# Kernel optimization log

Hardware: AMD Instinct MI355X
Metric: run time of the kernel (lower is better)

## Reference

```python
import jax, jax.numpy as jnp
import numpy as np

B, T, F, H = 16, 1024, 1024, 16
D = F // H  # 64

def setup_inputs() -> dict:
    key = jax.random.key(0)
    k0, k1, k2 = jax.random.split(key, 3)
    return {
        "x": jax.random.normal(k0, (B, T, F), jnp.float32),
        "mask": jnp.zeros((B, 1, T, 1), jnp.float32),
        "W_attn": jax.random.normal(k1, (F, 3 * F), jnp.float32) * 0.02,
        "b_attn": jnp.zeros((3 * F,), jnp.float32),
        "W_proj": jax.random.normal(k2, (F, F), jnp.float32) * 0.02,
        "b_proj": jnp.zeros((F,), jnp.float32),
    }

def reference(x, mask, W_attn, b_attn, W_proj, b_proj):
    # qkv projection (Conv1D == linear with transposed weight layout)
    qkv = x @ W_attn + b_attn                       # [B,T,3F]
    q, k, v = jnp.split(qkv, 3, axis=-1)
    split = lambda t: t.reshape(B, T, H, D).transpose(0, 2, 1, 3)  # [B,H,T,D]
    q, k, v = split(q), split(k), split(v)
    # non-standard: contract over T -> [B,H,D,D] score matrix
    s = jnp.einsum('bhtd,bhte->bhde', q, k) / jnp.sqrt(jnp.float32(D))
    tril = jnp.tril(jnp.ones((D, D), bool))         # bias buffer sliced to DxD
    s = jnp.where(tril, s, jnp.float32(-10000.0))
    # second matmul with V (before softmax), scaled by dk^2
    w = jnp.einsum('bhde,bhte->bhtd', s, v) / (jnp.float32(D) ** 2)  # [B,H,T,D]
    w = jax.nn.softmax(w + mask, axis=-2)           # softmax over T (dim=-2)
    a = w * v                                        # elementwise, not weighted sum
    merge = lambda t: t.transpose(0, 2, 1, 3).reshape(B, T, F)
    a = merge(a) @ W_proj + b_proj                   # output projection
    return a, merge(w)
```

## Files before the change

### kernel.cpp

```cpp
#include <hip/hip_runtime.h>
#include <math.h>

namespace {
constexpr int B = 16, T = 1024, F = 1024, H = 16, D = 64;
constexpr int NT = B * T;
constexpr int QKV_COLS = 3 * F;

constexpr size_t XHI_OFF = 0;
constexpr size_t XLO_OFF = 33554432;
constexpr size_t WAH_OFF = 67108864;
constexpr size_t WVL_OFF = 73400320;
constexpr size_t QB_OFF  = 75497472;
constexpr size_t KB_OFF  = 109051904;
constexpr size_t SB_OFF  = 142606336;
constexpr size_t AB_OFF  = 146800640;
constexpr size_t WPB_OFF = 180355072;
constexpr size_t VB_OFF   = QB_OFF;
constexpr size_t SP_OFF   = WVL_OFF;
}

typedef __attribute__((ext_vector_type(8))) __bf16 bf16x8;
typedef __attribute__((ext_vector_type(4))) float f32x4;

__device__ __forceinline__ unsigned short f2bf(float f) {
  unsigned u = __builtin_bit_cast(unsigned, f);
  u += 0x7FFFu + ((u >> 16) & 1u);
  return (unsigned short)(u >> 16);
}
__device__ __forceinline__ float bf2f(unsigned short s) {
  return __builtin_bit_cast(float, (unsigned)s << 16);
}
__device__ __forceinline__ void gld16(const unsigned short* g, unsigned short* l) {
  __builtin_amdgcn_global_load_lds(
      (const __attribute__((address_space(1))) unsigned int*)g,
      (__attribute__((address_space(3))) unsigned int*)l, 16, 0, 0);
}

__global__ __launch_bounds__(256) void cast_x(const float* __restrict__ x,
                                              unsigned short* __restrict__ xhi,
                                              unsigned short* __restrict__ xlo) {
  int i = (blockIdx.x * 256 + threadIdx.x) * 4;
  float4 v = *(const float4*)&x[i];
  ushort4 h, l;
  h.x = f2bf(v.x); l.x = f2bf(v.x - bf2f(h.x));
  h.y = f2bf(v.y); l.y = f2bf(v.y - bf2f(h.y));
  h.z = f2bf(v.z); l.z = f2bf(v.z - bf2f(h.z));
  h.w = f2bf(v.w); l.w = f2bf(v.w - bf2f(h.w));
  *(ushort4*)&xhi[i] = h;
  *(ushort4*)&xlo[i] = l;
}

__global__ __launch_bounds__(256) void tcast(const float* __restrict__ W,
                                             unsigned short* __restrict__ Wt,
                                             unsigned short* __restrict__ Wlo,
                                             int ncols, int locol0) {
  __shared__ float tile[64][65];
  const int bx = blockIdx.x, by = blockIdx.y, tid = threadIdx.x;
#pragma unroll
  for (int i = 0; i < 16; ++i) {
    int idx = tid + i * 256;
    int r = idx >> 6, c = idx & 63;
    tile[r][c] = W[(size_t)(by * 64 + r) * ncols + bx * 64 + c];
  }
  __syncthreads();
#pragma unroll
  for (int i = 0; i < 16; ++i) {
    int idx = tid + i * 256;
    int r = idx >> 6, c = idx & 63;
    int col = bx * 64 + r;
    float w = tile[c][r];
    unsigned short h = f2bf(w);
    Wt[(size_t)col * 1024 + by * 64 + c] = h;
    if (col >= locol0) {
      Wlo[(size_t)(col - locol0) * 1024 + by * 64 + c] = f2bf(w - bf2f(h));
    }
  }
}

__device__ __forceinline__ void stage256(const unsigned short* __restrict__ Ag,
                                         const unsigned short* __restrict__ Bg,
                                         int row0, int col0, int kin,
                                         unsigned short* lbase, int wave,
                                         int lane) {
  const int rsub = lane >> 3;
  const int logb = ((lane & 7) ^ rsub) << 4;
  const int isB = logb >> 6;
  const int koff = kin + ((logb & 63) >> 1);
#pragma unroll
  for (int L = 0; L < 4; ++L) {
    const int R0 = (L * 8 + wave) * 8;
    const int r = R0 + rsub;
    const unsigned short* src =
        isB ? (Bg + (size_t)(col0 + r) * 1024 + koff)
            : (Ag + (size_t)(row0 + r) * 1024 + koff);
    gld16(src, lbase + (size_t)R0 * 64);
  }
}

template <int MODE>
__device__ __forceinline__ void tile_src(
    int kt, const unsigned short* __restrict__ A0,
    const unsigned short* __restrict__ A1,
    const unsigned short* __restrict__ B0,
    const unsigned short* __restrict__ B1,
    const unsigned short*& Ag, const unsigned short*& Bg, int& kin) {
  if constexpr (MODE == 1) {
    const int seg = kt >> 5;
    kin = (kt & 31) << 5;
    Ag = (seg == 1) ? A1 : A0;
    Bg = (seg == 2) ? B1 : B0;
  } else {
    Ag = A0; Bg = B0; kin = kt << 5;
  }
}

__device__ __forceinline__ void read_frags(const char* tb, int wr, int wc,
                                           int m16, int quad,
                                           bf16x8 (&dst)[12]) {
#pragma unroll
  for (int j = 0; j < 4; ++j) {
    const int c = wc * 64 + j * 16 + m16;
    dst[j] = *(const bf16x8*)(tb + c * 128 +
                              ((64 + quad * 16) ^ ((c & 7) << 4)));
  }
#pragma unroll
  for (int i = 0; i < 8; ++i) {
    const int r = wr * 128 + i * 16 + m16;
    dst[4 + i] = *(const bf16x8*)(tb + r * 128 +
                                  ((quad * 16) ^ ((r & 7) << 4)));
  }
}

template <int MODE, int VM, bool STG, bool RDN>
__device__ __forceinline__ void half_body(
    int j, int row0, int col0, const unsigned short* __restrict__ A0,
    const unsigned short* __restrict__ A1,
    const unsigned short* __restrict__ B0,
    const unsigned short* __restrict__ B1,
    unsigned short (*lds)[256][64], int wave, int lane, int wr, int wc,
    int m16, int quad, bf16x8 (&cur)[12], bf16x8 (&nxt)[12],
    f32x4 (&acc)[8][4]) {
  if constexpr (STG) {
    const unsigned short *Ag, *Bg; int kin;
    tile_src<MODE>(j + 3, A0, A1, B0, B1, Ag, Bg, kin);
    stage256(Ag, Bg, row0, col0, kin, &lds[(j + 3) & 3][0][0], wave, lane);
  }
  if constexpr (VM == 8)      asm volatile("s_waitcnt vmcnt(8)" ::: "memory");
  else if constexpr (VM == 4) asm volatile("s_waitcnt vmcnt(4)" ::: "memory");
  else if constexpr (VM == 0) asm volatile("s_waitcnt vmcnt(0)" ::: "memory");
  __builtin_amdgcn_s_barrier();
  __builtin_amdgcn_sched_barrier(0);
  if constexpr (RDN) {
    read_frags((const char*)&lds[(j + 1) & 3][0][0], wr, wc, m16, quad, nxt);
  }
  __builtin_amdgcn_s_setprio(1);
#pragma unroll
  for (int i = 0; i < 8; ++i)
#pragma unroll
    for (int jj = 0; jj < 4; ++jj)
      acc[i][jj] = __builtin_amdgcn_mfma_f32_16x16x32_bf16(
          cur[4 + i], cur[jj], acc[i][jj], 0, 0, 0);
  __builtin_amdgcn_s_setprio(0);
  __builtin_amdgcn_s_barrier();
  __builtin_amdgcn_sched_barrier(0);
}

template <int MODE>
__global__ __launch_bounds__(512, 2) void gemm256(
    const unsigned short* __restrict__ A0, const unsigned short* __restrict__ A1,
    const unsigned short* __restrict__ B0, const unsigned short* __restrict__ B1,
    const float* __restrict__ bias, void* __restrict__ out0,
    void* __restrict__ out1) {
  __shared__ __align__(16) unsigned short lds[4][256][64];
  const int tid = threadIdx.x;
  const int wave = tid >> 6, lane = tid & 63;
  const int wr = wave >> 2, wc = wave & 3;
  const int m16 = lane & 15, quad = lane >> 4;
  const int row0 = blockIdx.y * 256, col0 = blockIdx.x * 256;
  constexpr int NKT = (MODE == 1) ? 96 : 32;
  f32x4 acc[8][4] = {};
  bf16x8 s0[12], s1[12];

#pragma unroll
  for (int p = 0; p < 3; ++p) {
    const unsigned short *Ag, *Bg; int kin;
    tile_src<MODE>(p, A0, A1, B0, B1, Ag, Bg, kin);
    stage256(Ag, Bg, row0, col0, kin, &lds[p][0][0], wave, lane);
  }
  asm volatile("s_waitcnt vmcnt(8)" ::: "memory");
  __builtin_amdgcn_s_barrier();
  __builtin_amdgcn_sched_barrier(0);
  read_frags((const char*)&lds[0][0][0], wr, wc, m16, quad, s0);

  int kt = 0;
  for (; kt + 5 < NKT; kt += 2) {
    half_body<MODE, 8, true, true>(kt, row0, col0, A0, A1, B0, B1, lds, wave,
                                   lane, wr, wc, m16, quad, s0, s1, acc);
    half_body<MODE, 8, true, true>(kt + 1, row0, col0, A0, A1, B0, B1, lds,
                                   wave, lane, wr, wc, m16, quad, s1, s0, acc);
  }
  half_body<MODE, 8, true, true>(NKT - 4, row0, col0, A0, A1, B0, B1, lds,
                                 wave, lane, wr, wc, m16, quad, s0, s1, acc);
  half_body<MODE, 4, false, true>(NKT - 3, row0, col0, A0, A1, B0, B1, lds,
                                  wave, lane, wr, wc, m16, quad, s1, s0, acc);
  half_body<MODE, 0, false, true>(NKT - 2, row0, col0, A0, A1, B0, B1, lds,
                                  wave, lane, wr, wc, m16, quad, s0, s1, acc);
  half_body<MODE, -1, false, false>(NKT - 1, row0, col0, A0, A1, B0, B1, lds,
                                    wave, lane, wr, wc, m16, quad, s1, s0, acc);

  if constexpr (MODE == 0) {
    unsigned short* dst = (col0 >= 1024) ? (unsigned short*)out1
                                         : (unsigned short*)out0;
#pragma unroll
    for (int j = 0; j < 4; ++j) {
      const int gcol = col0 + wc * 64 + j * 16 + m16;
      const int f = gcol & 1023;
      const int h = f >> 6, dd = f & 63;
      const float bv = bias[gcol];
#pragma unroll
      for (int i = 0; i < 8; ++i) {
#pragma unroll
        for (int r = 0; r < 4; ++r) {
          const int grow = row0 + wr * 128 + i * 16 + quad * 4 + r;
          const int b = grow >> 10, t = grow & 1023;
          dst[(((size_t)b * H + h) * T + t) * D + dd] = f2bf(acc[i][j][r] + bv);
        }
      }
    }
  } else if constexpr (MODE == 1) {
    float* vbp = (float*)out0;
#pragma unroll
    for (int j = 0; j < 4; ++j) {
      const int f = col0 + wc * 64 + j * 16 + m16;
      const int h = f >> 6, dd = f & 63;
      const float bv = bias[f];
#pragma unroll
      for (int i = 0; i < 8; ++i) {
#pragma unroll
        for (int r = 0; r < 4; ++r) {
          const int grow = row0 + wr * 128 + i * 16 + quad * 4 + r;
          const int b = grow >> 10, t = grow & 1023;
          vbp[(((size_t)b * H + h) * T + t) * D + dd] = acc[i][j][r] + bv;
        }
      }
    }
  } else {
    float* o = (float*)out0;
#pragma unroll
    for (int j = 0; j < 4; ++j) {
      const int gcol = col0 + wc * 64 + j * 16 + m16;
      const float bv = bias[gcol];
#pragma unroll
      for (int i = 0; i < 8; ++i) {
#pragma unroll
        for (int r = 0; r < 4; ++r) {
          const int grow = row0 + wr * 128 + i * 16 + quad * 4 + r;
          o[(size_t)grow * F + gcol] = acc[i][j][r] + bv;
        }
      }
    }
  }
}

__global__ __launch_bounds__(256) void score_kernel(
    const unsigned short* __restrict__ qb, const unsigned short* __restrict__ kb,
    float* __restrict__ sb) {
  __shared__ float qs[64][68];
  __shared__ float ks[64][68];
  const int bh = blockIdx.x;
  const int tid = threadIdx.x;
  const size_t base = (size_t)bh * T * D;
  const int d0 = (tid >> 4) * 4, e0 = (tid & 15) * 4;
  float acc[4][4] = {};
  for (int ch = 0; ch < T / 64; ++ch) {
#pragma unroll
    for (int i = 0; i < 4; ++i) {
      int idx = (tid + i * 256) * 4;
      ushort4 qv = *(const ushort4*)&qb[base + (size_t)ch * 4096 + idx];
      ushort4 kv = *(const ushort4*)&kb[base + (size_t)ch * 4096 + idx];
      int r = idx >> 6, c = idx & 63;
      float4 qf = make_float4(bf2f(qv.x), bf2f(qv.y), bf2f(qv.z), bf2f(qv.w));
      float4 kf = make_float4(bf2f(kv.x), bf2f(kv.y), bf2f(kv.z), bf2f(kv.w));
      *(float4*)&qs[r][c] = qf;
      *(float4*)&ks[r][c] = kf;
    }
    __syncthreads();
#pragma unroll 8
    for (int tt = 0; tt < 64; ++tt) {
      float4 qa4 = *(const float4*)&qs[tt][d0];
      float4 kv4 = *(const float4*)&ks[tt][e0];
      float qa[4] = {qa4.x, qa4.y, qa4.z, qa4.w};
      float kv[4] = {kv4.x, kv4.y, kv4.z, kv4.w};
#pragma unroll
      for (int i = 0; i < 4; ++i)
#pragma unroll
        for (int j = 0; j < 4; ++j) acc[i][j] += qa[i] * kv[j];
    }
    __syncthreads();
  }
#pragma unroll
  for (int i = 0; i < 4; ++i) {
#pragma unroll
    for (int j = 0; j < 4; ++j) {
      int dd = d0 + i, ee = e0 + j;
      float v = acc[i][j] * 0.125f;
      if (ee > dd) v = -10000.0f;
      sb[(size_t)bh * (D * D) + dd * D + ee] = v;
    }
  }
}

__global__ __launch_bounds__(256) void sum_kernel(
    const float* __restrict__ vb, const float* __restrict__ sb,
    const float* __restrict__ mask, float* __restrict__ sp) {
  const int tc = blockIdx.x, bh = blockIdx.y;
  const int b = bh >> 4;
  const int tid = threadIdx.x;
  const int lane = tid & 63;
  const int dg = __builtin_amdgcn_readfirstlane(tid >> 6);
  const int tg = tc * 64 + lane;
  const float* vrow = vb + (size_t)bh * (T * D) + (size_t)tg * D;
  float4 vreg[16];
#pragma unroll
  for (int i = 0; i < 16; ++i) vreg[i] = *(const float4*)&vrow[i * 4];
  const float mval = mask[(size_t)b * T + tg];
  float ex[16];
#pragma unroll
  for (int dd = 0; dd < 16; ++dd) {
    const int d = dg * 16 + dd;
    const float* srow = sb + (size_t)bh * 4096 + (size_t)d * 64;
    float acc = 0.f;
#pragma unroll
    for (int e4 = 0; e4 < 16; ++e4) {
      float4 s4 = *(const float4*)&srow[e4 * 4];
      acc += s4.x * vreg[e4].x + s4.y * vreg[e4].y +
             s4.z * vreg[e4].z + s4.w * vreg[e4].w;
    }
    float w = acc * (1.0f / 4096.0f) + mval;
    ex[dd] = __expf(w);
  }
#pragma unroll
  for (int dd = 0; dd < 16; ++dd) {
    float v = ex[dd];
    v += __shfl_xor(v, 1, 64);
    v += __shfl_xor(v, 2, 64);
    v += __shfl_xor(v, 4, 64);
    v += __shfl_xor(v, 8, 64);
    v += __shfl_xor(v, 16, 64);
    v += __shfl_xor(v, 32, 64);
    if (lane == 0) sp[((size_t)bh * 16 + tc) * 64 + dg * 16 + dd] = v;
  }
}

__global__ __launch_bounds__(256) void out_kernel(
    const float* __restrict__ vb, const float* __restrict__ sb,
    const float* __restrict__ mask, const float* __restrict__ sp,
    unsigned short* __restrict__ ab, float* __restrict__ out2) {
  __shared__ float olds[64][65];
  __shared__ float invS[64];
  const int tc = blockIdx.x, bh = blockIdx.y;
  const int b = bh >> 4, h = bh & 15;
  const int tid = threadIdx.x;
  if (tid < 64) {
    float S = 0.f;
#pragma unroll
    for (int j = 0; j < 16; ++j) S += sp[((size_t)bh * 16 + j) * 64 + tid];
    invS[tid] = 1.0f / S;
  }
  const int lane = tid & 63;
  const int dg = __builtin_amdgcn_readfirstlane(tid >> 6);
  const int tg = tc * 64 + lane;
  const float* vrow = vb + (size_t)bh * (T * D) + (size_t)tg * D;
  float4 vreg[16];
#pragma unroll
  for (int i = 0; i < 16; ++i) vreg[i] = *(const float4*)&vrow[i * 4];
  const float mval = mask[(size_t)b * T + tg];
#pragma unroll
  for (int dd = 0; dd < 16; ++dd) {
    const int d = dg * 16 + dd;
    const float* srow = sb + (size_t)bh * 4096 + (size_t)d * 64;
    float acc = 0.f;
#pragma unroll
    for (int e4 = 0; e4 < 16; ++e4) {
      float4 s4 = *(const float4*)&srow[e4 * 4];
      acc += s4.x * vreg[e4].x + s4.y * vreg[e4].y +
             s4.z * vreg[e4].z + s4.w * vreg[e4].w;
    }
    float w = acc * (1.0f / 4096.0f) + mval;
    olds[d][lane] = __expf(w);
  }
  __syncthreads();
  const int d = tid & 63, trow = tid >> 6;
  const float is = invS[d];
#pragma unroll
  for (int j = 0; j < 16; ++j) {
    int tl = trow * 16 + j;
    int tg2 = tc * 64 + tl;
    float o = olds[d][tl] * is;
    float vv = vb[(size_t)bh * (T * D) + (size_t)tg2 * D + d];
    size_t oidx = ((size_t)b * T + tg2) * F + h * 64 + d;
    out2[oidx] = o;
    ab[oidx] = f2bf(o * vv);
  }
}

extern "C" void kernel_launch(void* const* d_in, const int* in_sizes, int n_in,
                              void* d_out, int out_size, void* d_ws,
                              size_t ws_size, hipStream_t stream) {
  const float* x = (const float*)d_in[0];
  const float* mask = (const float*)d_in[1];
  const float* Wa = (const float*)d_in[2];
  const float* ba = (const float*)d_in[3];
  const float* Wp = (const float*)d_in[4];
  const float* bp = (const float*)d_in[5];
  char* ws = (char*)d_ws;
  float* out = (float*)d_out;

  unsigned short* xhi = (unsigned short*)(ws + XHI_OFF);
  unsigned short* xlo = (unsigned short*)(ws + XLO_OFF);
  unsigned short* Wah = (unsigned short*)(ws + WAH_OFF);
  unsigned short* Wvl = (unsigned short*)(ws + WVL_OFF);
  unsigned short* qb  = (unsigned short*)(ws + QB_OFF);
  unsigned short* kb  = (unsigned short*)(ws + KB_OFF);
  float* sb   = (float*)(ws + SB_OFF);
  unsigned short* ab  = (unsigned short*)(ws + AB_OFF);
  unsigned short* Wpb = (unsigned short*)(ws + WPB_OFF);
  float* vb   = (float*)(ws + VB_OFF);
  float* sp   = (float*)(ws + SP_OFF);

  cast_x<<<NT * F / 1024, 256, 0, stream>>>(x, xhi, xlo);
  tcast<<<dim3(QKV_COLS / 64, F / 64), 256, 0, stream>>>(Wa, Wah, Wvl,
                                                         QKV_COLS, 2048);
  tcast<<<dim3(F / 64, F / 64), 256, 0, stream>>>(Wp, Wpb, Wvl, F, 1 << 30);

  gemm256<0><<<dim3(2048 / 256, NT / 256), 512, 0, stream>>>(
      xhi, nullptr, Wah, nullptr, ba, qb, kb);

  score_kernel<<<dim3(B * H), 256, 0, stream>>>(qb, kb, sb);

  gemm256<1><<<dim3(F / 256, NT / 256), 512, 0, stream>>>(
      xhi, xlo, Wah + (size_t)2048 * 1024, Wvl, ba + 2048, vb, nullptr);

  sum_kernel<<<dim3(T / 64, B * H), 256, 0, stream>>>(vb, sb, mask, sp);

  out_kernel<<<dim3(T / 64, B * H), 256, 0, stream>>>(
      vb, sb, mask, sp, ab, out + (size_t)NT * F);

  gemm256<2><<<dim3(F / 256, NT / 256), 512, 0, stream>>>(
      ab, nullptr, Wpb, nullptr, bp, out, nullptr);
}
```

Measured before the change: 642.1 us.

## Fuse cast kernels into one prologue, add double-buffered QK GEMM, split score over T

Merges the x cast and both weight transpose-casts into a single prologue launch, cutting launch overhead and tail gaps. Replaces the MODE-0 QK projection with a dedicated qk_gemm that uses two LDS buffers (64 KB) and allows 4 blocks per CU instead of the 4-stage pipelined kernel. Doubles score_kernel's threads by splitting the T reduction into two halves and combining them through shared memory. The simpler QK GEMM pipeline may hide memory latency less well than the old 4-stage design, even with higher occupancy.

Result: slower. 1.192 ms (+85.7%).

```diff
diff --git a/kernel.cpp b/kernel.cpp
--- a/kernel.cpp
+++ b/kernel.cpp
@@ -36,26 +36,10 @@
       (__attribute__((address_space(3))) unsigned int*)l, 16, 0, 0);
 }
 
-__global__ __launch_bounds__(256) void cast_x(const float* __restrict__ x,
-                                              unsigned short* __restrict__ xhi,
-                                              unsigned short* __restrict__ xlo) {
-  int i = (blockIdx.x * 256 + threadIdx.x) * 4;
-  float4 v = *(const float4*)&x[i];
-  ushort4 h, l;
-  h.x = f2bf(v.x); l.x = f2bf(v.x - bf2f(h.x));
-  h.y = f2bf(v.y); l.y = f2bf(v.y - bf2f(h.y));
-  h.z = f2bf(v.z); l.z = f2bf(v.z - bf2f(h.z));
-  h.w = f2bf(v.w); l.w = f2bf(v.w - bf2f(h.w));
-  *(ushort4*)&xhi[i] = h;
-  *(ushort4*)&xlo[i] = l;
-}
-
-__global__ __launch_bounds__(256) void tcast(const float* __restrict__ W,
-                                             unsigned short* __restrict__ Wt,
-                                             unsigned short* __restrict__ Wlo,
-                                             int ncols, int locol0) {
-  __shared__ float tile[64][65];
-  const int bx = blockIdx.x, by = blockIdx.y, tid = threadIdx.x;
+__device__ __forceinline__ void tcast_body(
+    const float* __restrict__ W, unsigned short* __restrict__ Wt,
+    unsigned short* __restrict__ Wlo, int ncols, int locol0, int bx, int by,
+    int tid, float (*tile)[65]) {
 #pragma unroll
   for (int i = 0; i < 16; ++i) {
     int idx = tid + i * 256;
@@ -74,6 +58,33 @@
     if (col >= locol0) {
       Wlo[(size_t)(col - locol0) * 1024 + by * 64 + c] = f2bf(w - bf2f(h));
     }
+  }
+}
+
+__global__ __launch_bounds__(256) void prologue(
+    const float* __restrict__ x, unsigned short* __restrict__ xhi,
+    unsigned short* __restrict__ xlo, const float* __restrict__ Wa,
+    unsigned short* __restrict__ Wah, unsigned short* __restrict__ Wvl,
+    const float* __restrict__ Wp, unsigned short* __restrict__ Wpb) {
+  __shared__ float tile[64][65];
+  const int bid = blockIdx.x;
+  const int tid = threadIdx.x;
+  if (bid < 16384) {
+    int i = (bid * 256 + tid) * 4;
+    float4 v = *(const float4*)&x[i];
+    ushort4 h, l;
+    h.x = f2bf(v.x); l.x = f2bf(v.x - bf2f(h.x));
+    h.y = f2bf(v.y); l.y = f2bf(v.y - bf2f(h.y));
+    h.z = f2bf(v.z); l.z = f2bf(v.z - bf2f(h.z));
+    h.w = f2bf(v.w); l.w = f2bf(v.w - bf2f(h.w));
+    *(ushort4*)&xhi[i] = h;
+    *(ushort4*)&xlo[i] = l;
+  } else if (bid < 16384 + 768) {
+    int idx = bid - 16384;
+    tcast_body(Wa, Wah, Wvl, QKV_COLS, 2048, idx % 48, idx / 48, tid, tile);
+  } else {
+    int idx = bid - 16384 - 768;
+    tcast_body(Wp, Wpb, Wvl, F, 1 << 30, idx % 16, idx / 16, tid, tile);
   }
 }
 
@@ -131,6 +142,62 @@
   }
 }
 
+__global__ __launch_bounds__(512, 4) void qk_gemm(
+    const unsigned short* __restrict__ A, const unsigned short* __restrict__ Bt,
+    const float* __restrict__ ba, unsigned short* __restrict__ qb,
+    unsigned short* __restrict__ kb) {
+  __shared__ __align__(16) unsigned short lds[2][256][64];
+  const int tid = threadIdx.x;
+  const int wave = tid >> 6, lane = tid & 63;
+  const int wr = wave >> 2, wc = wave & 3;
+  const int m16 = lane & 15, quad = lane >> 4;
+  const int row0 = blockIdx.y * 256, col0 = blockIdx.x * 256;
+  f32x4 acc[8][4] = {};
+
+  stage256(A, Bt, row0, col0, 0, &lds[0][0][0], wave, lane);
+  for (int kt = 0; kt < 32; ++kt) {
+    if (kt + 1 < 32) {
+      stage256(A, Bt, row0, col0, (kt + 1) << 5, &lds[(kt + 1) & 1][0][0],
+               wave, lane);
+      asm volatile("s_waitcnt vmcnt(4)" ::: "memory");
+    } else {
+      asm volatile("s_waitcnt vmcnt(0)" ::: "memory");
+    }
+    __builtin_amdgcn_s_barrier();
+    __builtin_amdgcn_sched_barrier(0);
+    const char* tb = (const char*)&lds[kt & 1][0][0];
+    bf16x8 fr[12];
+    read_frags(tb, wr, wc, m16, quad, fr);
+    __builtin_amdgcn_s_setprio(1);
+#pragma unroll
+    for (int i = 0; i < 8; ++i)
+#pragma unroll
+      for (int j = 0; j < 4; ++j)
+        acc[i][j] = __builtin_amdgcn_mfma_f32_16x16x32_bf16(
+            fr[4 + i], fr[j], acc[i][j], 0, 0, 0);
+    __builtin_amdgcn_s_setprio(0);
+    __builtin_amdgcn_s_barrier();
+    __builtin_amdgcn_sched_barrier(0);
+  }
+  unsigned short* dst = (col0 >= 1024) ? kb : qb;
+#pragma unroll
+  for (int j = 0; j < 4; ++j) {
+    const int gcol = col0 + wc * 64 + j * 16 + m16;
+    const int f = gcol & 1023;
+    const int h = f >> 6, dd = f & 63;
+    const float bv = ba[gcol];
+#pragma unroll
+    for (int i = 0; i < 8; ++i) {
+#pragma unroll
+      for (int r = 0; r < 4; ++r) {
+        const int grow = row0 + wr * 128 + i * 16 + quad * 4 + r;
+        const int b = grow >> 10, t = grow & 1023;
+        dst[(((size_t)b * H + h) * T + t) * D + dd] = f2bf(acc[i][j][r] + bv);
+      }
+    }
+  }
+}
+
 template <int MODE, int VM, bool STG, bool RDN>
 __device__ __forceinline__ void half_body(
     int j, int row0, int col0, const unsigned short* __restrict__ A0,
@@ -169,8 +236,7 @@
 __global__ __launch_bounds__(512, 2) void gemm256(
     const unsigned short* __restrict__ A0, const unsigned short* __restrict__ A1,
     const unsigned short* __restrict__ B0, const unsigned short* __restrict__ B1,
-    const float* __restrict__ bias, void* __restrict__ out0,
-    void* __restrict__ out1) {
+    const float* __restrict__ bias, void* __restrict__ out0) {
   __shared__ __align__(16) unsigned short lds[4][256][64];
   const int tid = threadIdx.x;
   const int wave = tid >> 6, lane = tid & 63;
@@ -208,26 +274,7 @@
   half_body<MODE, -1, false, false>(NKT - 1, row0, col0, A0, A1, B0, B1, lds,
                                     wave, lane, wr, wc, m16, quad, s1, s0, acc);
 
-  if constexpr (MODE == 0) {
-    unsigned short* dst = (col0 >= 1024) ? (unsigned short*)out1
-                                         : (unsigned short*)out0;
-#pragma unroll
-    for (int j = 0; j < 4; ++j) {
-      const int gcol = col0 + wc * 64 + j * 16 + m16;
-      const int f = gcol & 1023;
-      const int h = f >> 6, dd = f & 63;
-      const float bv = bias[gcol];
-#pragma unroll
-      for (int i = 0; i < 8; ++i) {
-#pragma unroll
-        for (int r = 0; r < 4; ++r) {
-          const int grow = row0 + wr * 128 + i * 16 + quad * 4 + r;
-          const int b = grow >> 10, t = grow & 1023;
-          dst[(((size_t)b * H + h) * T + t) * D + dd] = f2bf(acc[i][j][r] + bv);
-        }
-      }
-    }
-  } else if constexpr (MODE == 1) {
+  if constexpr (MODE == 1) {
     float* vbp = (float*)out0;
 #pragma unroll
     for (int j = 0; j < 4; ++j) {
@@ -262,31 +309,33 @@
   }
 }
 
-__global__ __launch_bounds__(256) void score_kernel(
+__global__ __launch_bounds__(512) void score_kernel(
     const unsigned short* __restrict__ qb, const unsigned short* __restrict__ kb,
     float* __restrict__ sb) {
   __shared__ float qs[64][68];
   __shared__ float ks[64][68];
   const int bh = blockIdx.x;
   const int tid = threadIdx.x;
+  const int inner = tid & 255, half = tid >> 8;
   const size_t base = (size_t)bh * T * D;
-  const int d0 = (tid >> 4) * 4, e0 = (tid & 15) * 4;
+  const int d0 = (inner >> 4) * 4, e0 = (inner & 15) * 4;
+  const int t0 = half * 32;
   float acc[4][4] = {};
   for (int ch = 0; ch < T / 64; ++ch) {
 #pragma unroll
-    for (int i = 0; i < 4; ++i) {
-      int idx = (tid + i * 256) * 4;
+    for (int i = 0; i < 2; ++i) {
+      int idx = (tid + i * 512) * 4;
       ushort4 qv = *(const ushort4*)&qb[base + (size_t)ch * 4096 + idx];
       ushort4 kv = *(const ushort4*)&kb[base + (size_t)ch * 4096 + idx];
       int r = idx >> 6, c = idx & 63;
-      float4 qf = make_float4(bf2f(qv.x), bf2f(qv.y), bf2f(qv.z), bf2f(qv.w));
-      float4 kf = make_float4(bf2f(kv.x), bf2f(kv.y), bf2f(kv.z), bf2f(kv.w));
-      *(float4*)&qs[r][c] = qf;
-      *(float4*)&ks[r][c] = kf;
+      *(float4*)&qs[r][c] =
+          make_float4(bf2f(qv.x), bf2f(qv.y), bf2f(qv.z), bf2f(qv.w));
+      *(float4*)&ks[r][c] =
+          make_float4(bf2f(kv.x), bf2f(kv.y), bf2f(kv.z), bf2f(kv.w));
     }
     __syncthreads();
 #pragma unroll 8
-    for (int tt = 0; tt < 64; ++tt) {
+    for (int tt = t0; tt < t0 + 32; ++tt) {
       float4 qa4 = *(const float4*)&qs[tt][d0];
       float4 kv4 = *(const float4*)&ks[tt][e0];
       float qa[4] = {qa4.x, qa4.y, qa4.z, qa4.w};
@@ -298,14 +347,25 @@
     }
     __syncthreads();
   }
-#pragma unroll
-  for (int i = 0; i < 4; ++i) {
-#pragma unroll
-    for (int j = 0; j < 4; ++j) {
-      int dd = d0 + i, ee = e0 + j;
-      float v = acc[i][j] * 0.125f;
-      if (ee > dd) v = -10000.0f;
-      sb[(size_t)bh * (D * D) + dd * D + ee] = v;
+  float* scratch = &qs[0][0];
+  if (half == 1) {
+#pragma unroll
+    for (int i = 0; i < 4; ++i)
+#pragma unroll
+      for (int j = 0; j < 4; ++j)
+        scratch[inner * 16 + i * 4 + j] = acc[i][j];
+  }
+  __syncthreads();
+  if (half == 0) {
+#pragma unroll
+    for (int i = 0; i < 4; ++i) {
+#pragma unroll
+      for (int j = 0; j < 4; ++j) {
+        int dd = d0 + i, ee = e0 + j;
+        float v = (acc[i][j] + scratch[inner * 16 + i * 4 + j]) * 0.125f;
+        if (ee > dd) v = -10000.0f;
+        sb[(size_t)bh * (D * D) + dd * D + ee] = v;
+      }
     }
   }
 }
@@ -428,18 +488,15 @@
   float* vb   = (float*)(ws + VB_OFF);
   float* sp   = (float*)(ws + SP_OFF);
 
-  cast_x<<<NT * F / 1024, 256, 0, stream>>>(x, xhi, xlo);
-  tcast<<<dim3(QKV_COLS / 64, F / 64), 256, 0, stream>>>(Wa, Wah, Wvl,
-                                                         QKV_COLS, 2048);
-  tcast<<<dim3(F / 64, F / 64), 256, 0, stream>>>(Wp, Wpb, Wvl, F, 1 << 30);
-
-  gemm256<0><<<dim3(2048 / 256, NT / 256), 512, 0, stream>>>(
-      xhi, nullptr, Wah, nullptr, ba, qb, kb);
-
-  score_kernel<<<dim3(B * H), 256, 0, stream>>>(qb, kb, sb);
+  prologue<<<16384 + 768 + 256, 256, 0, stream>>>(x, xhi, xlo, Wa, Wah, Wvl,
+                                                  Wp, Wpb);
+
+  qk_gemm<<<dim3(2048 / 256, NT / 256), 512, 0, stream>>>(xhi, Wah, ba, qb, kb);
+
+  score_kernel<<<dim3(B * H), 512, 0, stream>>>(qb, kb, sb);
 
   gemm256<1><<<dim3(F / 256, NT / 256), 512, 0, stream>>>(
-      xhi, xlo, Wah + (size_t)2048 * 1024, Wvl, ba + 2048, vb, nullptr);
+      xhi, xlo, Wah + (size_t)2048 * 1024, Wvl, ba + 2048, vb);
 
   sum_kernel<<<dim3(T / 64, B * H), 256, 0, stream>>>(vb, sb, mask, sp);
 
@@ -447,5 +504,5 @@
       vb, sb, mask, sp, ab, out + (size_t)NT * F);
 
   gemm256<2><<<dim3(F / 256, NT / 256), 512, 0, stream>>>(
-      ab, nullptr, Wpb, nullptr, bp, out, nullptr);
-}
+      ab, nullptr, Wpb, nullptr, bp, out);
+}
```
